# Optimization experiments

Measured on AMD Instinct MI355X. Metric: run time of the kernel, lower is better.

The kernel has to match this reference:

```python
import jax, jax.numpy as jnp
import numpy as np

N, M, C = 16384, 4096, 32
R = 2.0            # max_neighbour_distance
MULT = 2.0         # neighbor_distance_multiplier
NV = 3             # voxels per axis
TV = NV * NV * NV  # 27 total grid voxels
CH = 128           # query chunk size for kNN
EPS_D = 1e-8
BN_EPS = 1e-5


def _grid_offsets():
    g = jnp.linspace(-R + R / NV, R - R / NV, NV)
    x, y, z = jnp.meshgrid(g, g, g, indexing='ij')
    return jnp.stack([x.ravel(), y.ravel(), z.ravel()], axis=-1)  # (27,3)


def _three_nn(support_xyz, new_xyz, grid_centers):
    """3-NN of each grid center among support points within a cube of half-width
    MULT*R around the parent keypoint (two-step search, neighbor_type=0 cube).
    Returns squared dists (M,27,3), idx (M,27,3), empty (M,)."""
    q = new_xyz.reshape(-1, CH, 3)
    g = grid_centers.reshape(-1, CH, TV, 3)

    def body(args):
        qc, gc = args                                   # (CH,3), (CH,27,3)
        diff = jnp.abs(support_xyz[None, :, :] - qc[:, None, :])   # (CH,N,3)
        cand = jnp.max(diff, axis=-1) <= MULT * R                   # (CH,N)
        d2 = jnp.sum((gc[:, :, None, :] - support_xyz[None, None, :, :]) ** 2,
                     axis=-1)                                       # (CH,27,N)
        d2 = jnp.where(cand[:, None, :], d2, jnp.inf)
        nd, idx = jax.lax.top_k(-d2, 3)                              # (CH,27,3)
        return -nd, idx, ~jnp.any(cand, axis=-1)

    d3, idx, empty = jax.lax.map(body, (q, g))
    d3 = jnp.where(jnp.isinf(d3), 1e10, d3)  # <3 candidates -> ~zero weight
    return (d3.reshape(-1, TV, 3), idx.reshape(-1, TV, 3), empty.reshape(-1))


def _bn_relu(x, gamma, beta):
    mu = jnp.mean(x, axis=0)
    var = jnp.var(x, axis=0)
    return jax.nn.relu((x - mu) * jax.lax.rsqrt(var + BN_EPS) * gamma + beta)


def _forward(support_xyz, support_features, new_xyz,
             w1, bn1_gamma, bn1_beta, w2, bn2_gamma, bn2_beta):
    grid_centers = new_xyz[:, None, :] + _grid_offsets()[None, :, :]  # (M,27,3)
    d3, idx, empty = _three_nn(support_xyz, new_xyz, grid_centers)
    d3 = jax.lax.stop_gradient(d3)  # torch computes kNN under no_grad

    dist_recip = 1.0 / (d3 + EPS_D)                                   # (M,27,3)
    norm = jnp.sum(dist_recip, axis=-1, keepdims=True)
    weight = dist_recip / jnp.maximum(norm, 1e-8)

    nbr_feats = support_features[idx]                 # (M,27,3,C) gather
    interp = jnp.einsum('mgk,mgkc->mgc', weight, nbr_feats)          # (M,27,C)

    nbr_xyz = support_xyz[idx]                        # (M,27,3,3)
    local_xyz = (grid_centers[:, :, None, :] - nbr_xyz).reshape(M, TV, 9)
    feats = jnp.concatenate([interp, local_xyz], axis=-1)            # (M,27,C+9)
    feats = jnp.where(empty[:, None, None], 0.0, feats)

    # grouped Conv1d (kernel 1, groups=27): per-voxel matmul
    y = jnp.einsum('mgc,goc->mgo', feats, w1).reshape(M, TV * 32)     # (M,864)
    y = _bn_relu(y, bn1_gamma, bn1_beta)
    z = y @ w2.T                                                      # (M,128)
    return _bn_relu(z, bn2_gamma, bn2_beta)


def setup_inputs() -> dict:
    key = jax.random.key(0)
    ks = jax.random.split(key, 5)
    scale = jnp.array([50.0, 50.0, 4.0])
    shift = jnp.array([0.0, 0.0, -2.0])
    support_xyz = jax.random.uniform(ks[0], (N, 3)) * scale + shift
    new_xyz = jax.random.uniform(ks[1], (M, 3)) * scale + shift
    support_features = jax.random.normal(ks[2], (N, C))
    w1 = jax.random.normal(ks[3], (TV, 32, C + 9)) * (2.0 / (C + 9)) ** 0.5
    w2 = jax.random.normal(ks[4], (128, TV * 32)) * (2.0 / (TV * 32)) ** 0.5
    return {
        'support_xyz': support_xyz,
        'support_features': support_features,
        'new_xyz': new_xyz,
        'w1': w1,
        'bn1_gamma': jnp.ones(TV * 32),
        'bn1_beta': jnp.zeros(TV * 32),
        'w2': w2,
        'bn2_gamma': jnp.ones(128),
        'bn2_beta': jnp.zeros(128),
    }


def reference(support_xyz, support_features, new_xyz,
              w1, bn1_gamma, bn1_beta, w2, bn2_gamma, bn2_beta):
    return _forward(support_xyz, support_features, new_xyz,
                    w1, bn1_gamma, bn1_beta, w2, bn2_gamma, bn2_beta)
```

## Files before the change

### kernel.cpp

```cpp
#include <hip/hip_runtime.h>
#include <hip/hip_bf16.h>

#define N_SUP 16384
#define M_Q   4096
#define TV    27
#define CIN   41
#define CH1   864
#define CH2   128
#define CAP   1024
#define NB    12

#define KC_BK  24
#define KC_KS  216
#define KC_NCH 4

__device__ __forceinline__ float gsel(int i){
  const float GOFF = (float)(-2.0 + 2.0 / 3.0);
  return (i == 0) ? GOFF : ((i == 2) ? -GOFF : 0.0f);
}

__device__ __forceinline__ int binOf(float x){
  int b = (int)(x * (float)(NB / 50.0));
  return (b < 0) ? 0 : ((b > NB - 1) ? NB - 1 : b);
}

__device__ __forceinline__ void insK(unsigned long long key,
                                     unsigned long long& k0,
                                     unsigned long long& k1,
                                     unsigned long long& k2){
  bool b0 = key < k0, b1 = key < k1, b2 = key < k2;
  k2 = b1 ? k1 : (b2 ? key : k2);
  k1 = b0 ? k0 : (b1 ? key : k1);
  k0 = b0 ? key : k0;
}

__global__ void kPre(const float* __restrict__ w1, float* __restrict__ w1T,
                     const float* __restrict__ w2, float* __restrict__ w2T,
                     const float* __restrict__ sup_xyz, int* __restrict__ counts)
{
  int idx = blockIdx.x * 256 + threadIdx.x;
  if (idx < N_SUP) {
    float x = sup_xyz[3*idx], y = sup_xyz[3*idx+1];
    atomicAdd(&counts[binOf(x) * NB + binOf(y)], 1);
  }
  if (idx < CIN * CH1) {
    int k = idx / CH1, t = idx % CH1;
    w1T[idx] = w1[(size_t)t * CIN + k];
  }
  int j = idx - CIN * CH1;
  if (j >= 0 && j < CH1 * CH2) {
    int k = j / CH2, c = j % CH2;
    w2T[j] = w2[(size_t)c * CH1 + k];
  }
}

__global__ void kScan(const int* __restrict__ counts, int* __restrict__ starts, int* __restrict__ cursor)
{
  __shared__ int sc[NB*NB];
  int t = threadIdx.x;
  if (t < NB*NB) sc[t] = counts[t];
  __syncthreads();
  if (t == 0) {
    int acc = 0;
    for (int b = 0; b < NB*NB; b++) { int c = sc[b]; sc[b] = acc; acc += c; }
  }
  __syncthreads();
  if (t < NB*NB) { starts[t] = sc[t]; cursor[t] = sc[t]; }
  if (t == NB*NB) starts[NB*NB] = N_SUP;
}

__global__ void kScatter(const float* __restrict__ sup_xyz, int* __restrict__ cursor,
                         float* __restrict__ xs, float* __restrict__ ys,
                         float* __restrict__ zs, int* __restrict__ sid)
{
  int i = blockIdx.x * 256 + threadIdx.x;
  if (i < N_SUP) {
    float x = sup_xyz[3*i], y = sup_xyz[3*i+1], z = sup_xyz[3*i+2];
    int b = binOf(x) * NB + binOf(y);
    int p = atomicAdd(&cursor[b], 1);
    xs[p] = x; ys[p] = y; zs[p] = z; sid[p] = i;
  }
}

__global__ __launch_bounds__(256) void kA12(const float* __restrict__ xs,
                                            const float* __restrict__ ys,
                                            const float* __restrict__ zs,
                                            const int*   __restrict__ sid,
                                            const int*   __restrict__ starts,
                                            const float* __restrict__ new_xyz,
                                            float* __restrict__ nnD,
                                            int*   __restrict__ nnGI)
{
  __shared__ float4 cxyz[CAP];
  __shared__ unsigned long long sk[TV][8][3];
  __shared__ int s_cnt;

  const int m   = blockIdx.x;
  const int tid = threadIdx.x;
  if (tid == 0) s_cnt = 0;
  __syncthreads();

  const float qx = new_xyz[m*3+0];
  const float qy = new_xyz[m*3+1];
  const float qz = new_xyz[m*3+2];

  const int bx0 = binOf(qx - 4.0f), bx1 = binOf(qx + 4.0f);
  const int by0 = binOf(qy - 4.0f), by1 = binOf(qy + 4.0f);
  for (int bx = bx0; bx <= bx1; bx++) {
    const int beg = starts[bx * NB + by0];
    const int end = starts[bx * NB + by1 + 1];
    for (int i = beg + tid; i < end; i += 256) {
      float x = xs[i], y = ys[i];
      if (fabsf(__fsub_rn(x, qx)) <= 4.0f && fabsf(__fsub_rn(y, qy)) <= 4.0f) {
        int p = atomicAdd(&s_cnt, 1);
        if (p < CAP) cxyz[p] = make_float4(x, y, zs[i], __uint_as_float((unsigned)sid[i]));
      }
    }
  }
  __syncthreads();
  const int cnt = (s_cnt < CAP) ? s_cnt : CAP;

  const int v = tid >> 3, j = tid & 7;
  if (v < TV) {
    const float gx = qx + gsel(v / 9);
    const float gy = qy + gsel((v / 3) % 3);
    const float gz = qz + gsel(v % 3);
    unsigned long long k0 = ~0ull, k1 = ~0ull, k2 = ~0ull;
    float k2df = __uint_as_float(0xFFFFFFFFu);
    for (int c = j; c < cnt; c += 8) {
      float4 f4 = cxyz[c];
      float dx = __fsub_rn(gx, f4.x);
      float dy = __fsub_rn(gy, f4.y);
      float dz = __fsub_rn(gz, f4.z);
      float dd = __fadd_rn(__fadd_rn(__fmul_rn(dx,dx), __fmul_rn(dy,dy)), __fmul_rn(dz,dz));
      if (!(dd > k2df)) {
        unsigned long long key = ((unsigned long long)__float_as_uint(dd) << 32)
                               | (unsigned long long)__float_as_uint(f4.w);
        insK(key, k0, k1, k2);
        k2df = __uint_as_float((unsigned)(k2 >> 32));
      }
    }
    sk[v][j][0] = k0; sk[v][j][1] = k1; sk[v][j][2] = k2;
  }
  __syncthreads();

  if (tid < TV) {
    const int vv = tid;
    unsigned long long k0 = ~0ull, k1 = ~0ull, k2 = ~0ull;
    #pragma unroll
    for (int jj = 0; jj < 8; jj++) {
      insK(sk[vv][jj][0], k0, k1, k2);
      insK(sk[vv][jj][1], k0, k1, k2);
      insK(sk[vv][jj][2], k0, k1, k2);
    }
    const int base = m * TV + vv;
    if (cnt > 0) {
      unsigned long long ks[3] = {k0, k1, k2};
      #pragma unroll
      for (int r = 0; r < 3; r++) {
        unsigned db = (unsigned)(ks[r] >> 32);
        bool ok = (db != 0xFFFFFFFFu);
        nnD[base*3+r]  = ok ? __uint_as_float(db) : 1e10f;
        nnGI[base*3+r] = ok ? (int)(unsigned)(ks[r] & 0xFFFFFFFFull) : 0;
      }
    } else {
      #pragma unroll
      for (int r = 0; r < 3; r++) { nnD[base*3+r] = -1.0f; nnGI[base*3+r] = 0; }
    }
  }
}

__global__ __launch_bounds__(256) void kA3(const float* __restrict__ sup_feat,
                                           const float* __restrict__ sup_xyz,
                                           const float* __restrict__ new_xyz,
                                           const float* __restrict__ nnD,
                                           const int*   __restrict__ nnGI,
                                           const float* __restrict__ w1T,
                                           float* __restrict__ y1,
                                           float* __restrict__ stats1)
{
  __shared__ float s_feats[4][TV][CIN];
  __shared__ float s_w[4][TV][3];
  __shared__ int   s_gi[4][TV][3];

  const int m0  = blockIdx.x * 4;
  const int tid = threadIdx.x;

  if (tid < 4*TV) {
    const int q = tid / TV, vv = tid % TV;
    const int m = m0 + q;
    const int base = m * TV + vv;
    float d[3]; int gi[3];
    #pragma unroll
    for (int r = 0; r < 3; r++) { d[r] = nnD[base*3+r]; gi[r] = nnGI[base*3+r]; }
    #pragma unroll
    for (int r = 0; r < 3; r++) s_gi[q][vv][r] = gi[r];
    if (d[0] < 0.0f) {
      #pragma unroll
      for (int r = 0; r < 3; r++) s_w[q][vv][r] = 0.0f;
      #pragma unroll
      for (int jj = 0; jj < 9; jj++) s_feats[q][vv][32 + jj] = 0.0f;
    } else {
      float r0 = 1.0f / (d[0] + 1e-8f);
      float r1 = 1.0f / (d[1] + 1e-8f);
      float r2 = 1.0f / (d[2] + 1e-8f);
      float den = fmaxf(r0 + r1 + r2, 1e-8f);
      s_w[q][vv][0] = r0 / den; s_w[q][vv][1] = r1 / den; s_w[q][vv][2] = r2 / den;
      const float gx = new_xyz[m*3+0] + gsel(vv / 9);
      const float gy = new_xyz[m*3+1] + gsel((vv / 3) % 3);
      const float gz = new_xyz[m*3+2] + gsel(vv % 3);
      #pragma unroll
      for (int r = 0; r < 3; r++) {
        bool ok = (d[r] != 1e10f);
        s_feats[q][vv][32 + r*3 + 0] = ok ? (gx - sup_xyz[gi[r]*3 + 0]) : 0.0f;
        s_feats[q][vv][32 + r*3 + 1] = ok ? (gy - sup_xyz[gi[r]*3 + 1]) : 0.0f;
        s_feats[q][vv][32 + r*3 + 2] = ok ? (gz - sup_xyz[gi[r]*3 + 2]) : 0.0f;
      }
    }
  }
  __syncthreads();

  for (int t = tid; t < 4*TV*32; t += 256) {
    const int q = t / (TV*32), rem = t % (TV*32);
    const int v = rem >> 5, ch = rem & 31;
    s_feats[q][v][ch] = s_w[q][v][0] * sup_feat[s_gi[q][v][0]*32 + ch]
                      + s_w[q][v][1] * sup_feat[s_gi[q][v][1]*32 + ch]
                      + s_w[q][v][2] * sup_feat[s_gi[q][v][2]*32 + ch];
  }
  __syncthreads();

  const int copy = (blockIdx.x & 7) * 2 * CH1;
  for (int t = tid; t < CH1; t += 256) {
    const int v = t >> 5;
    float acc[4];
    #pragma unroll
    for (int q = 0; q < 4; q++) acc[q] = 0.0f;
    for (int k = 0; k < CIN; k++) {
      float w = w1T[k * CH1 + t];
      #pragma unroll
      for (int q = 0; q < 4; q++) acc[q] += s_feats[q][v][k] * w;
    }
    float s = 0.0f, ss = 0.0f;
    #pragma unroll
    for (int q = 0; q < 4; q++) {
      y1[(size_t)(m0 + q) * CH1 + t] = acc[q];
      s += acc[q]; ss += acc[q] * acc[q];
    }
    atomicAdd(&stats1[copy + t],       s);
    atomicAdd(&stats1[copy + CH1 + t], ss);
  }
}

__global__ __launch_bounds__(256) void kC(const float* __restrict__ y1,
                                          const float* __restrict__ stats1,
                                          const float* __restrict__ g1,
                                          const float* __restrict__ b1,
                                          const float* __restrict__ w2T,
                                          float* __restrict__ zpart)
{
  __shared__ float As[KC_BK][36];
  __shared__ float Bs[KC_BK][CH2];
  __shared__ float lsc[KC_KS], lsh[KC_KS];

  const int tid = threadIdx.x;
  const int mb  = blockIdx.x & 127;
  const int ch  = blockIdx.x >> 7;
  const int m0  = mb * 32;
  const int kb  = ch * KC_KS;

  for (int t = tid; t < KC_KS; t += 256) {
    const int c = kb + t;
    float s = 0.0f, ssq = 0.0f;
    #pragma unroll
    for (int k = 0; k < 8; k++) {
      s   += stats1[k * 2 * CH1 + c];
      ssq += stats1[k * 2 * CH1 + CH1 + c];
    }
    float mu  = s  * (1.0f / M_Q);
    float var = ssq * (1.0f / M_Q) - mu * mu;
    float r   = 1.0f / sqrtf(var + 1e-5f);
    float gg = g1[c];
    lsc[t] = r * gg;
    lsh[t] = b1[c] - mu * r * gg;
  }

  const int ar = tid >> 3;
  const int ac = (tid & 7) * 3;
  const int ty = tid >> 5;
  const int tx = tid & 31;

  float pa0, pa1, pa2; float4 pb[3];
  {
    const float* yr = &y1[(size_t)(m0 + ar) * CH1 + kb + ac];
    pa0 = yr[0]; pa1 = yr[1]; pa2 = yr[2];
    #pragma unroll
    for (int jj = 0; jj < 3; jj++) {
      int fid = tid + jj * 256; int kk = fid >> 5, c4 = (fid & 31) * 4;
      pb[jj] = *(const float4*)&w2T[(size_t)(kb + kk) * CH2 + c4];
    }
  }

  float acc[4][4];
  #pragma unroll
  for (int i = 0; i < 4; i++)
    #pragma unroll
    for (int jj = 0; jj < 4; jj++) acc[i][jj] = 0.0f;

  for (int kt = 0; kt < KC_KS / KC_BK; kt++) {
    __syncthreads();
    const int kl = kt * KC_BK + ac;
    As[ac  ][ar] = fmaxf(pa0 * lsc[kl  ] + lsh[kl  ], 0.0f);
    As[ac+1][ar] = fmaxf(pa1 * lsc[kl+1] + lsh[kl+1], 0.0f);
    As[ac+2][ar] = fmaxf(pa2 * lsc[kl+2] + lsh[kl+2], 0.0f);
    #pragma unroll
    for (int jj = 0; jj < 3; jj++) {
      int fid = tid + jj * 256; int kk = fid >> 5, c4 = (fid & 31) * 4;
      *(float4*)&Bs[kk][c4] = pb[jj];
    }
    __syncthreads();
    if (kt + 1 < KC_KS / KC_BK) {
      const float* yr = &y1[(size_t)(m0 + ar) * CH1 + kb + (kt+1) * KC_BK + ac];
      pa0 = yr[0]; pa1 = yr[1]; pa2 = yr[2];
      #pragma unroll
      for (int jj = 0; jj < 3; jj++) {
        int fid = tid + jj * 256; int kk = fid >> 5, c4 = (fid & 31) * 4;
        pb[jj] = *(const float4*)&w2T[(size_t)(kb + (kt+1) * KC_BK + kk) * CH2 + c4];
      }
    }
    #pragma unroll
    for (int kk = 0; kk < KC_BK; kk++) {
      float4 av = *(const float4*)&As[kk][ty*4];
      float4 bv = *(const float4*)&Bs[kk][tx*4];
      acc[0][0] += av.x*bv.x; acc[0][1] += av.x*bv.y; acc[0][2] += av.x*bv.z; acc[0][3] += av.x*bv.w;
      acc[1][0] += av.y*bv.x; acc[1][1] += av.y*bv.y; acc[1][2] += av.y*bv.z; acc[1][3] += av.y*bv.w;
      acc[2][0] += av.z*bv.x; acc[2][1] += av.z*bv.y; acc[2][2] += av.z*bv.z; acc[2][3] += av.z*bv.w;
      acc[3][0] += av.w*bv.x; acc[3][1] += av.w*bv.y; acc[3][2] += av.w*bv.z; acc[3][3] += av.w*bv.w;
    }
  }

  float* zp = zpart + (size_t)ch * M_Q * CH2;
  #pragma unroll
  for (int i = 0; i < 4; i++) {
    *(float4*)&zp[(size_t)(m0 + ty*4 + i) * CH2 + tx*4] =
        make_float4(acc[i][0], acc[i][1], acc[i][2], acc[i][3]);
  }
}

__global__ void kZ(const float* __restrict__ zpart,
                   float* __restrict__ z,
                   float* __restrict__ stats2)
{
  const int tid = threadIdx.x;
  const int c = tid & 127, h = tid >> 7;
  const int m0 = blockIdx.x * 8 + h * 4;
  float s = 0.0f, ss = 0.0f;
  for (int r = 0; r < 4; r++) {
    size_t off = (size_t)(m0 + r) * CH2 + c;
    float v = zpart[off]
            + zpart[off + (size_t)M_Q*CH2]
            + zpart[off + (size_t)2*M_Q*CH2]
            + zpart[off + (size_t)3*M_Q*CH2];
    z[off] = v;
    s += v; ss += v * v;
  }
  const int copy = (blockIdx.x & 7) * 256;
  atomicAdd(&stats2[copy + c],       s);
  atomicAdd(&stats2[copy + 128 + c], ss);
}

__global__ void kD(const float* __restrict__ z,
                   const float* __restrict__ stats2,
                   const float* __restrict__ g2,
                   const float* __restrict__ b2,
                   float* __restrict__ out)
{
  int t4 = blockIdx.x * 256 + threadIdx.x;
  if (t4 >= M_Q * CH2 / 4) return;
  int c = (t4 & 31) * 4;
  float4 zv = *(const float4*)&z[(size_t)t4 * 4];
  float4 sv = make_float4(0,0,0,0), qv = make_float4(0,0,0,0);
  #pragma unroll
  for (int k = 0; k < 8; k++) {
    float4 a = *(const float4*)&stats2[k * 256 + c];
    float4 b = *(const float4*)&stats2[k * 256 + 128 + c];
    sv.x += a.x; sv.y += a.y; sv.z += a.z; sv.w += a.w;
    qv.x += b.x; qv.y += b.y; qv.z += b.z; qv.w += b.w;
  }
  float4 gv = *(const float4*)&g2[c];
  float4 bv = *(const float4*)&b2[c];
  float4 o;
  {
    float mu = sv.x * (1.0f/M_Q), var = qv.x * (1.0f/M_Q) - mu*mu;
    o.x = fmaxf((zv.x - mu) * (1.0f/sqrtf(var + 1e-5f)) * gv.x + bv.x, 0.0f);
  }
  {
    float mu = sv.y * (1.0f/M_Q), var = qv.y * (1.0f/M_Q) - mu*mu;
    o.y = fmaxf((zv.y - mu) * (1.0f/sqrtf(var + 1e-5f)) * gv.y + bv.y, 0.0f);
  }
  {
    float mu = sv.z * (1.0f/M_Q), var = qv.z * (1.0f/M_Q) - mu*mu;
    o.z = fmaxf((zv.z - mu) * (1.0f/sqrtf(var + 1e-5f)) * gv.z + bv.z, 0.0f);
  }
  {
    float mu = sv.w * (1.0f/M_Q), var = qv.w * (1.0f/M_Q) - mu*mu;
    o.w = fmaxf((zv.w - mu) * (1.0f/sqrtf(var + 1e-5f)) * gv.w + bv.w, 0.0f);
  }
  *(float4*)&out[(size_t)t4 * 4] = o;
}

extern "C" void kernel_launch(void* const* d_in, const int* in_sizes, int n_in,
                              void* d_out, int out_size, void* d_ws, size_t ws_size,
                              hipStream_t stream)
{
  const float* sup_xyz  = (const float*)d_in[0];
  const float* sup_feat = (const float*)d_in[1];
  const float* new_xyz  = (const float*)d_in[2];
  const float* w1       = (const float*)d_in[3];
  const float* g1       = (const float*)d_in[4];
  const float* b1       = (const float*)d_in[5];
  const float* w2       = (const float*)d_in[6];
  const float* g2       = (const float*)d_in[7];
  const float* b2       = (const float*)d_in[8];
  float* out = (float*)d_out;

  char* ws = (char*)d_ws;
  float* y1     = (float*)(ws);
  float* z      = (float*)(ws + 14155776);
  float* w2T    = (float*)(ws + 16252928);
  float* stats1 = (float*)(ws + 16695296);
  float* stats2 = (float*)(ws + 16750592);
  int*   counts = (int*)  (ws + 16758784);
  int*   cursor = (int*)  (ws + 16759360);
  int*   starts = (int*)  (ws + 16759936);
  float* xs     = (float*)(ws + 16760516);
  float* ys     = (float*)(ws + 16826052);
  float* zs     = (float*)(ws + 16891588);
  int*   sid    = (int*)  (ws + 16957124);
  float* nnD    = (float*)(ws + 17022660);
  int*   nnGI   = (int*)  (ws + 18349764);
  float* zpart  = (float*)(ws + 17022660);
  float* w1T    = z;

  hipMemsetAsync(stats1, 0, 55296 + 8192 + 576 + 576, stream);

  const int PRE_TOT = CIN*CH1 + CH1*CH2;
  hipLaunchKernelGGL(kPre,    dim3((PRE_TOT + 255) / 256), dim3(256), 0, stream, w1, w1T, w2, w2T, sup_xyz, counts);
  hipLaunchKernelGGL(kScan,   dim3(1),                    dim3(256), 0, stream, counts, starts, cursor);
  hipLaunchKernelGGL(kScatter,dim3((N_SUP + 255) / 256),  dim3(256), 0, stream, sup_xyz, cursor, xs, ys, zs, sid);
  hipLaunchKernelGGL(kA12,    dim3(M_Q),                  dim3(256), 0, stream, xs, ys, zs, sid, starts, new_xyz, nnD, nnGI);
  hipLaunchKernelGGL(kA3,     dim3(M_Q / 4),              dim3(256), 0, stream, sup_feat, sup_xyz, new_xyz, nnD, nnGI, w1T, y1, stats1);
  hipLaunchKernelGGL(kC,      dim3(128 * KC_NCH),         dim3(256), 0, stream, y1, stats1, g1, b1, w2T, zpart);
  hipLaunchKernelGGL(kZ,      dim3(M_Q / 8),              dim3(256), 0, stream, zpart, z, stats2);
  hipLaunchKernelGGL(kD,      dim3(M_Q * CH2 / 4 / 256),  dim3(256), 0, stream, z, stats2, g2, b2, out);
}
```

Measured before the change: 144.9 us.

## Pack binned support points as float4, use 9 kNN lanes per voxel, 8 queries per kA3 block

The scatter kernel now writes each binned support point as one float4 (x, y, z, original index) instead of four separate arrays. The kNN gather kernel then loads a single 16-byte record per candidate and stores it straight into shared memory. The per-voxel kNN search is split across 9 lanes instead of 8, so 243 of the 256 threads are busy rather than 216. The layer-1 kernel handles 8 queries per block instead of 4, reusing each w1T load across more queries at the cost of more registers and shared memory.

```diff
diff --git a/kernel.cpp b/kernel.cpp
--- a/kernel.cpp
+++ b/kernel.cpp
@@ -9,6 +9,7 @@
 #define CH2   128
 #define CAP   1024
 #define NB    12
+#define NSL   9
 
 #define KC_BK  24
 #define KC_KS  216
@@ -70,29 +71,25 @@
 }
 
 __global__ void kScatter(const float* __restrict__ sup_xyz, int* __restrict__ cursor,
-                         float* __restrict__ xs, float* __restrict__ ys,
-                         float* __restrict__ zs, int* __restrict__ sid)
+                         float4* __restrict__ pxyzs)
 {
   int i = blockIdx.x * 256 + threadIdx.x;
   if (i < N_SUP) {
     float x = sup_xyz[3*i], y = sup_xyz[3*i+1], z = sup_xyz[3*i+2];
     int b = binOf(x) * NB + binOf(y);
     int p = atomicAdd(&cursor[b], 1);
-    xs[p] = x; ys[p] = y; zs[p] = z; sid[p] = i;
-  }
-}
-
-__global__ __launch_bounds__(256) void kA12(const float* __restrict__ xs,
-                                            const float* __restrict__ ys,
-                                            const float* __restrict__ zs,
-                                            const int*   __restrict__ sid,
+    pxyzs[p] = make_float4(x, y, z, __uint_as_float((unsigned)i));
+  }
+}
+
+__global__ __launch_bounds__(256) void kA12(const float4* __restrict__ pxyzs,
                                             const int*   __restrict__ starts,
                                             const float* __restrict__ new_xyz,
                                             float* __restrict__ nnD,
                                             int*   __restrict__ nnGI)
 {
   __shared__ float4 cxyz[CAP];
-  __shared__ unsigned long long sk[TV][8][3];
+  __shared__ unsigned long long sk[TV][NSL][3];
   __shared__ int s_cnt;
 
   const int m   = blockIdx.x;
@@ -110,24 +107,24 @@
     const int beg = starts[bx * NB + by0];
     const int end = starts[bx * NB + by1 + 1];
     for (int i = beg + tid; i < end; i += 256) {
-      float x = xs[i], y = ys[i];
-      if (fabsf(__fsub_rn(x, qx)) <= 4.0f && fabsf(__fsub_rn(y, qy)) <= 4.0f) {
+      float4 pt = pxyzs[i];
+      if (fabsf(__fsub_rn(pt.x, qx)) <= 4.0f && fabsf(__fsub_rn(pt.y, qy)) <= 4.0f) {
         int p = atomicAdd(&s_cnt, 1);
-        if (p < CAP) cxyz[p] = make_float4(x, y, zs[i], __uint_as_float((unsigned)sid[i]));
+        if (p < CAP) cxyz[p] = pt;
       }
     }
   }
   __syncthreads();
   const int cnt = (s_cnt < CAP) ? s_cnt : CAP;
 
-  const int v = tid >> 3, j = tid & 7;
+  const int v = tid / NSL, j = tid % NSL;
   if (v < TV) {
     const float gx = qx + gsel(v / 9);
     const float gy = qy + gsel((v / 3) % 3);
     const float gz = qz + gsel(v % 3);
     unsigned long long k0 = ~0ull, k1 = ~0ull, k2 = ~0ull;
     float k2df = __uint_as_float(0xFFFFFFFFu);
-    for (int c = j; c < cnt; c += 8) {
+    for (int c = j; c < cnt; c += NSL) {
       float4 f4 = cxyz[c];
       float dx = __fsub_rn(gx, f4.x);
       float dy = __fsub_rn(gy, f4.y);
@@ -148,7 +145,7 @@
     const int vv = tid;
     unsigned long long k0 = ~0ull, k1 = ~0ull, k2 = ~0ull;
     #pragma unroll
-    for (int jj = 0; jj < 8; jj++) {
+    for (int jj = 0; jj < NSL; jj++) {
       insK(sk[vv][jj][0], k0, k1, k2);
       insK(sk[vv][jj][1], k0, k1, k2);
       insK(sk[vv][jj][2], k0, k1, k2);
@@ -179,14 +176,14 @@
                                            float* __restrict__ y1,
                                            float* __restrict__ stats1)
 {
-  __shared__ float s_feats[4][TV][CIN];
-  __shared__ float s_w[4][TV][3];
-  __shared__ int   s_gi[4][TV][3];
-
-  const int m0  = blockIdx.x * 4;
+  __shared__ float s_feats[8][TV][CIN];
+  __shared__ float s_w[8][TV][3];
+  __shared__ int   s_gi[8][TV][3];
+
+  const int m0  = blockIdx.x * 8;
   const int tid = threadIdx.x;
 
-  if (tid < 4*TV) {
+  if (tid < 8*TV) {
     const int q = tid / TV, vv = tid % TV;
     const int m = m0 + q;
     const int base = m * TV + vv;
@@ -220,7 +217,7 @@
   }
   __syncthreads();
 
-  for (int t = tid; t < 4*TV*32; t += 256) {
+  for (int t = tid; t < 8*TV*32; t += 256) {
     const int q = t / (TV*32), rem = t % (TV*32);
     const int v = rem >> 5, ch = rem & 31;
     s_feats[q][v][ch] = s_w[q][v][0] * sup_feat[s_gi[q][v][0]*32 + ch]
@@ -232,17 +229,17 @@
   const int copy = (blockIdx.x & 7) * 2 * CH1;
   for (int t = tid; t < CH1; t += 256) {
     const int v = t >> 5;
-    float acc[4];
-    #pragma unroll
-    for (int q = 0; q < 4; q++) acc[q] = 0.0f;
+    float acc[8];
+    #pragma unroll
+    for (int q = 0; q < 8; q++) acc[q] = 0.0f;
     for (int k = 0; k < CIN; k++) {
       float w = w1T[k * CH1 + t];
       #pragma unroll
-      for (int q = 0; q < 4; q++) acc[q] += s_feats[q][v][k] * w;
+      for (int q = 0; q < 8; q++) acc[q] += s_feats[q][v][k] * w;
     }
     float s = 0.0f, ss = 0.0f;
     #pragma unroll
-    for (int q = 0; q < 4; q++) {
+    for (int q = 0; q < 8; q++) {
       y1[(size_t)(m0 + q) * CH1 + t] = acc[q];
       s += acc[q]; ss += acc[q] * acc[q];
     }
@@ -424,31 +421,28 @@
   float* out = (float*)d_out;
 
   char* ws = (char*)d_ws;
-  float* y1     = (float*)(ws);
-  float* z      = (float*)(ws + 14155776);
-  float* w2T    = (float*)(ws + 16252928);
-  float* stats1 = (float*)(ws + 16695296);
-  float* stats2 = (float*)(ws + 16750592);
-  int*   counts = (int*)  (ws + 16758784);
-  int*   cursor = (int*)  (ws + 16759360);
-  int*   starts = (int*)  (ws + 16759936);
-  float* xs     = (float*)(ws + 16760516);
-  float* ys     = (float*)(ws + 16826052);
-  float* zs     = (float*)(ws + 16891588);
-  int*   sid    = (int*)  (ws + 16957124);
-  float* nnD    = (float*)(ws + 17022660);
-  int*   nnGI   = (int*)  (ws + 18349764);
-  float* zpart  = (float*)(ws + 17022660);
-  float* w1T    = z;
+  float*  y1     = (float*)(ws);
+  float*  z      = (float*)(ws + 14155776);
+  float*  w2T    = (float*)(ws + 16252928);
+  float*  stats1 = (float*)(ws + 16695296);
+  float*  stats2 = (float*)(ws + 16750592);
+  int*    counts = (int*)  (ws + 16758784);
+  int*    cursor = (int*)  (ws + 16759360);
+  int*    starts = (int*)  (ws + 16759936);
+  float4* pxyzs  = (float4*)(ws + 16760528);
+  float*  nnD    = (float*)(ws + 17022672);
+  int*    nnGI   = (int*)  (ws + 18349776);
+  float*  zpart  = (float*)(ws + 17022672);
+  float*  w1T    = z;
 
   hipMemsetAsync(stats1, 0, 55296 + 8192 + 576 + 576, stream);
 
   const int PRE_TOT = CIN*CH1 + CH1*CH2;
   hipLaunchKernelGGL(kPre,    dim3((PRE_TOT + 255) / 256), dim3(256), 0, stream, w1, w1T, w2, w2T, sup_xyz, counts);
   hipLaunchKernelGGL(kScan,   dim3(1),                    dim3(256), 0, stream, counts, starts, cursor);
-  hipLaunchKernelGGL(kScatter,dim3((N_SUP + 255) / 256),  dim3(256), 0, stream, sup_xyz, cursor, xs, ys, zs, sid);
-  hipLaunchKernelGGL(kA12,    dim3(M_Q),                  dim3(256), 0, stream, xs, ys, zs, sid, starts, new_xyz, nnD, nnGI);
-  hipLaunchKernelGGL(kA3,     dim3(M_Q / 4),              dim3(256), 0, stream, sup_feat, sup_xyz, new_xyz, nnD, nnGI, w1T, y1, stats1);
+  hipLaunchKernelGGL(kScatter,dim3((N_SUP + 255) / 256),  dim3(256), 0, stream, sup_xyz, cursor, pxyzs);
+  hipLaunchKernelGGL(kA12,    dim3(M_Q),                  dim3(256), 0, stream, pxyzs, starts, new_xyz, nnD, nnGI);
+  hipLaunchKernelGGL(kA3,     dim3(M_Q / 8),              dim3(256), 0, stream, sup_feat, sup_xyz, new_xyz, nnD, nnGI, w1T, y1, stats1);
   hipLaunchKernelGGL(kC,      dim3(128 * KC_NCH),         dim3(256), 0, stream, y1, stats1, g1, b1, w2T, zpart);
   hipLaunchKernelGGL(kZ,      dim3(M_Q / 8),              dim3(256), 0, stream, zpart, z, stats2);
   hipLaunchKernelGGL(kD,      dim3(M_Q * CH2 / 4 / 256),  dim3(256), 0, stream, z, stats2, g2, b2, out);
```

Result: faster. 140.1 us (-3.3%).
